# Performance work log

Hardware: AMD Instinct MI355X
Metric: run time of the kernel (lower is better)

Reference implementation:

```python
import jax, jax.numpy as jnp
import numpy as np

HEADS = 16

def _layernorm_LC(x, eps=1e-05):
    # Normalizes jointly over the last TWO dims (L, C), matching the custom LayerNorm.
    mean = jnp.mean(x, axis=(-2, -1), keepdims=True)
    var = jnp.mean((x - mean) ** 2, axis=(-2, -1), keepdims=True) + eps
    return (x - mean) / jnp.sqrt(var)  # affine is identity (ones/zeros)


def setup_inputs() -> dict:
    key = jax.random.key(0)
    ks = jax.random.split(key, 11)
    B, L, D = 2, 2048, 1024
    H = 4 * D
    s = 0.02
    return {
        'x': jax.random.normal(ks[0], (B, L, D), jnp.float32),
        'wq': jax.random.normal(ks[1], (D, D), jnp.float32) * s,
        'bq': jax.random.normal(ks[2], (D,), jnp.float32) * s,
        'wk': jax.random.normal(ks[3], (D, D), jnp.float32) * s,
        'bk': jax.random.normal(ks[4], (D,), jnp.float32) * s,
        'wv': jax.random.normal(ks[5], (D, D), jnp.float32) * s,
        'bv': jax.random.normal(ks[6], (D,), jnp.float32) * s,
        'w1': jax.random.normal(ks[7], (D, H), jnp.float32) * s,
        'b1': jax.random.normal(ks[8], (H,), jnp.float32) * s,
        'w2': jax.random.normal(ks[9], (H, D), jnp.float32) * s,
        'b2': jax.random.normal(ks[10], (D,), jnp.float32) * s,
    }


def reference(x, wq, bq, wk, bk, wv, bv, w1, b1, w2, b2):
    B, L, D = x.shape
    dh = D // HEADS
    # QKV projections
    q = (x @ wq + bq).reshape(B, L, HEADS, dh)
    k = (x @ wk + bk).reshape(B, L, HEADS, dh)
    v = (x @ wv + bv).reshape(B, L, HEADS, dh)
    # batched multi-head attention (equivalent to the per-head Python loop)
    scale = 1.0 / jnp.sqrt(jnp.float32(dh))
    scores = jnp.einsum('blhd,bmhd->bhlm', q, k) * scale
    attn = jax.nn.softmax(scores, axis=-1)
    out = jnp.einsum('bhlm,bmhd->blhd', attn, v).reshape(B, L, D)
    # residual + (L,C) layernorm
    h = _layernorm_LC(x + out)
    # feedforward (dropout is identity in eval)
    ff = jax.nn.relu(h @ w1 + b1) @ w2 + b2
    return _layernorm_LC(h + ff)
```

## Files before the change

### kernel.cpp

```cpp
#include <hip/hip_runtime.h>
#include <hip/hip_bf16.h>

typedef __hip_bfloat16 bf16;
typedef __attribute__((ext_vector_type(8))) short short8;
typedef __attribute__((ext_vector_type(4))) short short4v;
typedef __attribute__((ext_vector_type(4))) float f32x4;

#define CB 2
#define CL 2048
#define CD 1024
#define CH 4096
#define NHEADS 16
#define DH 64

__device__ __forceinline__ short f2bs(float f) {
    __hip_bfloat16 h = __float2bfloat16(f);
    return *reinterpret_cast<short*>(&h);
}
__device__ __forceinline__ float bs2f(short s) {
    __hip_bfloat16 h = *reinterpret_cast<__hip_bfloat16*>(&s);
    return __bfloat162float(h);
}

__device__ __forceinline__ void async_copy16(const short* g, short* l) {
    __builtin_amdgcn_global_load_lds((const __attribute__((address_space(1))) unsigned int*)g,
                                     (__attribute__((address_space(3))) unsigned int*)l,
                                     16, 0, 0);
}

__global__ void pack_bias_kernel(const float* __restrict__ bq, const float* __restrict__ bk,
                                 const float* __restrict__ bv, float* __restrict__ o,
                                 float* __restrict__ stats) {
    int i = blockIdx.x * 256 + threadIdx.x;
    if (i < 16) stats[i] = 0.0f;
    if (i < 3072) o[i] = i < 1024 ? bq[i] : (i < 2048 ? bk[i - 1024] : bv[i - 2048]);
}

__global__ void cvt_x_kernel(const float* __restrict__ x, short* __restrict__ o) {
    const int i = (blockIdx.x * 256 + threadIdx.x) * 4;
    const float4 v = *(const float4*)&x[i];
    short4v s; s[0] = f2bs(v.x); s[1] = f2bs(v.y); s[2] = f2bs(v.z); s[3] = f2bs(v.w);
    *(short4v*)&o[i] = s;
}

__global__ void transpose_cvt(const float* __restrict__ in, short* __restrict__ out,
                              int K, int N, int row_off) {
    __shared__ float T[32][33];
    const int tx = threadIdx.x & 31, ty = threadIdx.x >> 5;
    const int k0 = blockIdx.y * 32, n0 = blockIdx.x * 32;
    #pragma unroll
    for (int i = 0; i < 4; ++i)
        T[ty + i * 8][tx] = in[(size_t)(k0 + ty + i * 8) * N + n0 + tx];
    __syncthreads();
    #pragma unroll
    for (int i = 0; i < 4; ++i)
        out[(size_t)(row_off + n0 + ty + i * 8) * K + k0 + tx] = f2bs(T[tx][ty + i * 8]);
}

__global__ void transpose_qkv(const float* __restrict__ wq, const float* __restrict__ wk,
                              const float* __restrict__ wv, short* __restrict__ out) {
    __shared__ float T[32][33];
    const int z = blockIdx.z;
    const float* in = z == 0 ? wq : (z == 1 ? wk : wv);
    const int row_off = z * 1024;
    const int tx = threadIdx.x & 31, ty = threadIdx.x >> 5;
    const int k0 = blockIdx.y * 32, n0 = blockIdx.x * 32;
    #pragma unroll
    for (int i = 0; i < 4; ++i)
        T[ty + i * 8][tx] = in[(size_t)(k0 + ty + i * 8) * CD + n0 + tx];
    __syncthreads();
    #pragma unroll
    for (int i = 0; i < 4; ++i)
        out[(size_t)(row_off + n0 + ty + i * 8) * CD + k0 + tx] = f2bs(T[tx][ty + i * 8]);
}

template <int BN, int BK, int RELU, int EPI>
__launch_bounds__(256)
__global__ void gemm_mfma(const short* __restrict__ A,
                          const short* __restrict__ Bt,
                          const float* __restrict__ bias,
                          short* __restrict__ C,
                          short* __restrict__ C2,
                          int M, int N, int K,
                          float* __restrict__ stats) {
    constexpr int NT = BN / 32;
    constexpr int KH = BK / 32;
    constexpr int ACH = 16 * BK;
    constexpr int BCH = BN * BK / 8;
    __shared__ short As[128 * BK];
    __shared__ short Bs[BN * BK];
    __shared__ float red[8];

    const int tid = threadIdx.x;
    const int wave = tid >> 6, lane = tid & 63, quad = lane >> 4, lm = lane & 15;
    const int wm = (wave & 1) * 64, wn = (wave >> 1) * (NT * 16);

    const int id = blockIdx.y * gridDim.x + blockIdx.x;
    const int xcd = id & 7, within = id >> 3;
    const int by = xcd * 4 + (within & 3);
    const int bx = within >> 2;
    const int row0 = by * 128, col0 = bx * BN;

    f32x4 acc[4][NT];
    #pragma unroll
    for (int i = 0; i < 4; ++i)
        #pragma unroll
        for (int j = 0; j < NT; ++j) { f32x4 z = {0.f, 0.f, 0.f, 0.f}; acc[i][j] = z; }

    for (int k0 = 0; k0 < K; k0 += BK) {
        #pragma unroll
        for (int t = 0; t < ACH / 256; ++t) {
            const int c = t * 256 + tid;
            const int slab = c >> 9, idx = c & 511;
            const int r = idx >> 2, seg = idx & 3;
            async_copy16(A + (size_t)(row0 + r) * K + k0 + slab * 32 + seg * 8, &As[c * 8]);
        }
        #pragma unroll
        for (int t = 0; t < BCH / 256; ++t) {
            const int c = t * 256 + tid;
            const int slab = c / (BN * 4), idx = c % (BN * 4);
            const int r = idx >> 2, seg = idx & 3;
            async_copy16(Bt + (size_t)(col0 + r) * K + k0 + slab * 32 + seg * 8, &Bs[c * 8]);
        }
        __syncthreads();

        #pragma unroll
        for (int kh = 0; kh < KH; ++kh) {
            short8 af[4], bfr[NT];
            #pragma unroll
            for (int mt = 0; mt < 4; ++mt)
                af[mt] = *(const short8*)&As[kh * 4096 + (wm + mt * 16 + lm) * 32 + quad * 8];
            #pragma unroll
            for (int nt = 0; nt < NT; ++nt)
                bfr[nt] = *(const short8*)&Bs[kh * (BN * 32) + (wn + nt * 16 + lm) * 32 + quad * 8];
            #pragma unroll
            for (int mt = 0; mt < 4; ++mt)
                #pragma unroll
                for (int nt = 0; nt < NT; ++nt)
                    acc[mt][nt] = __builtin_amdgcn_mfma_f32_16x16x32_bf16(af[mt], bfr[nt], acc[mt][nt], 0, 0, 0);
        }
        __syncthreads();
    }

    float s1 = 0.f, s2 = 0.f;
    #pragma unroll
    for (int mt = 0; mt < 4; ++mt) {
        #pragma unroll
        for (int nt = 0; nt < NT; ++nt) {
            const int col = col0 + wn + nt * 16 + lm;
            const float bv = bias[col];
            const int rowb = row0 + wm + mt * 16 + quad * 4;
            if (EPI == 1 && col >= 2048) {
                const int b = row0 >> 11;
                const int l0 = rowb & (CL - 1);
                short4v sv;
                #pragma unroll
                for (int r = 0; r < 4; ++r) sv[r] = f2bs(acc[mt][nt][r] + bv);
                *(short4v*)&C2[(size_t)b * CD * CL + (size_t)(col - 2048) * CL + l0] = sv;
            } else {
                #pragma unroll
                for (int r = 0; r < 4; ++r) {
                    float v = acc[mt][nt][r] + bv;
                    if (RELU) v = fmaxf(v, 0.f);
                    const int ld = (EPI == 1) ? 2048 : N;
                    const size_t idx = (size_t)(rowb + r) * ld + col;
                    if (EPI == 2) {
                        v += bs2f(C[idx]);
                        s1 += v; s2 += v * v;
                    }
                    C[idx] = f2bs(v);
                }
            }
        }
    }
    if (EPI == 2) {
        #pragma unroll
        for (int off = 1; off <= 32; off <<= 1) {
            s1 += __shfl_xor(s1, off, 64);
            s2 += __shfl_xor(s2, off, 64);
        }
        if (lane == 0) { red[wave] = s1; red[4 + wave] = s2; }
        __syncthreads();
        if (tid == 0) {
            const int batch = row0 >> 11;
            atomicAdd(&stats[batch * 2 + 0], red[0] + red[1] + red[2] + red[3]);
            atomicAdd(&stats[batch * 2 + 1], red[4] + red[5] + red[6] + red[7]);
        }
    }
}

__launch_bounds__(256)
__global__ void attn_mfma(const short* __restrict__ qk,
                          const short* __restrict__ vT,
                          const float* __restrict__ x,
                          short* __restrict__ sbuf,
                          float* __restrict__ stats) {
    __shared__ short Ks[2][64 * 64];
    __shared__ short Vs[2][64 * 64];
    __shared__ float red[8];

    const int tid = threadIdx.x;
    const int wave = tid >> 6, lane = tid & 63, quad = lane >> 4, lm = lane & 15;
    const int sx = lm & 7;

    const int id = blockIdx.z * (16 * 16) + blockIdx.y * 16 + blockIdx.x;
    const int xcd = id & 7, rest = id >> 3;
    const int qx = rest & 15, gq = rest >> 4;
    const int g = gq * 8 + xcd;
    const int h = g & 15, b = g >> 4;

    const int hoff = h * DH;
    const size_t rowb = (size_t)b * CL;
    const size_t vbase = (size_t)b * CD * CL + (size_t)hoff * CL;
    const int qbase0 = qx * 128 + wave * 32;

    short8 bq[2][2];
    #pragma unroll
    for (int qt = 0; qt < 2; ++qt)
        #pragma unroll
        for (int kf = 0; kf < 2; ++kf)
            bq[qt][kf] = *(const short8*)(qk + (rowb + qbase0 + qt * 16 + lm) * 2048 + hoff + kf * 32 + quad * 8);

    f32x4 oacc[2][4];
    #pragma unroll
    for (int qt = 0; qt < 2; ++qt)
        #pragma unroll
        for (int mt = 0; mt < 4; ++mt) { f32x4 z = {0.f, 0.f, 0.f, 0.f}; oacc[qt][mt] = z; }
    float lsum[2] = {0.f, 0.f};

    auto stage = [&](int buf, int kt) {
        #pragma unroll
        for (int t = 0; t < 2; ++t) {
            const int c = tid + t * 256;
            const int key = c >> 3, sp = c & 7;
            async_copy16(qk + (rowb + kt * 64 + key) * 2048 + 1024 + hoff + ((sp ^ (key & 7)) * 8),
                         &Ks[buf][c * 8]);
        }
        #pragma unroll
        for (int t = 0; t < 2; ++t) {
            const int c = tid + t * 256;
            const int row = c >> 3, sp = c & 7;
            async_copy16(vT + vbase + (size_t)row * CL + kt * 64 + ((sp ^ (row & 7)) * 8),
                         &Vs[buf][c * 8]);
        }
    };

    stage(0, 0);
    __syncthreads();
    int cur = 0;

    for (int kt = 0; kt < CL / 64; ++kt) {
        if (kt + 1 < CL / 64) stage(cur ^ 1, kt + 1);
        const short* K_ = &Ks[cur][0];
        const short* V_ = &Vs[cur][0];

        float st[2][4][4];
        #pragma unroll
        for (int ktile = 0; ktile < 4; ++ktile) {
            const int krow = ktile * 16 + lm;
            const int s0 = (quad ^ sx) << 3;
            const short8 a0 = *(const short8*)&K_[krow * 64 + s0];
            const short8 a1 = *(const short8*)&K_[krow * 64 + (s0 ^ 32)];
            f32x4 sv[2];
            __builtin_amdgcn_s_setprio(1);
            #pragma unroll
            for (int qt = 0; qt < 2; ++qt) {
                f32x4 s = {0.f, 0.f, 0.f, 0.f};
                s = __builtin_amdgcn_mfma_f32_16x16x32_bf16(a0, bq[qt][0], s, 0, 0, 0);
                s = __builtin_amdgcn_mfma_f32_16x16x32_bf16(a1, bq[qt][1], s, 0, 0, 0);
                sv[qt] = s;
            }
            __builtin_amdgcn_s_setprio(0);
            #pragma unroll
            for (int qt = 0; qt < 2; ++qt)
                #pragma unroll
                for (int r = 0; r < 4; ++r) {
                    const float p = __expf(sv[qt][r] * 0.125f);
                    lsum[qt] += p;
                    st[qt][ktile][r] = p;
                }
        }

        #pragma unroll
        for (int p = 0; p < 2; ++p) {
            short8 pf[2];
            #pragma unroll
            for (int qt = 0; qt < 2; ++qt)
                #pragma unroll
                for (int r = 0; r < 4; ++r) {
                    pf[qt][r]     = f2bs(st[qt][2 * p][r]);
                    pf[qt][4 + r] = f2bs(st[qt][2 * p + 1][r]);
                }
            #pragma unroll
            for (int mt = 0; mt < 4; ++mt) {
                const int vrow = mt * 16 + lm;
                const int sc = (p * 4 + (quad >> 1)) ^ sx;
                const int vb = vrow * 64 + (quad & 1) * 4;
                const short4v vlo = *(const short4v*)&V_[vb + sc * 8];
                const short4v vhi = *(const short4v*)&V_[vb + (sc ^ 2) * 8];
                short8 vf;
                vf[0] = vlo[0]; vf[1] = vlo[1]; vf[2] = vlo[2]; vf[3] = vlo[3];
                vf[4] = vhi[0]; vf[5] = vhi[1]; vf[6] = vhi[2]; vf[7] = vhi[3];
                __builtin_amdgcn_s_setprio(1);
                #pragma unroll
                for (int qt = 0; qt < 2; ++qt)
                    oacc[qt][mt] = __builtin_amdgcn_mfma_f32_16x16x32_bf16(vf, pf[qt], oacc[qt][mt], 0, 0, 0);
                __builtin_amdgcn_s_setprio(0);
            }
        }
        __syncthreads();
        cur ^= 1;
    }

    #pragma unroll
    for (int qt = 0; qt < 2; ++qt) {
        lsum[qt] += __shfl_xor(lsum[qt], 16, 64);
        lsum[qt] += __shfl_xor(lsum[qt], 32, 64);
    }

    float s1 = 0.f, s2 = 0.f;
    #pragma unroll
    for (int qt = 0; qt < 2; ++qt) {
        const float inv = 1.0f / lsum[qt];
        const size_t grow = rowb + qbase0 + qt * 16 + lm;
        #pragma unroll
        for (int mt = 0; mt < 4; ++mt) {
            const size_t base = grow * CD + hoff + mt * 16 + quad * 4;
            const float4 xv = *(const float4*)&x[base];
            const float xa[4] = {xv.x, xv.y, xv.z, xv.w};
            short4v sv;
            #pragma unroll
            for (int r = 0; r < 4; ++r) {
                const float s = xa[r] + oacc[qt][mt][r] * inv;
                s1 += s; s2 += s * s;
                sv[r] = f2bs(s);
            }
            *(short4v*)&sbuf[base] = sv;
        }
    }
    #pragma unroll
    for (int off = 1; off <= 32; off <<= 1) {
        s1 += __shfl_xor(s1, off, 64);
        s2 += __shfl_xor(s2, off, 64);
    }
    if (lane == 0) { red[wave] = s1; red[4 + wave] = s2; }
    __syncthreads();
    if (tid == 0) {
        atomicAdd(&stats[b * 2 + 0], red[0] + red[1] + red[2] + red[3]);
        atomicAdd(&stats[b * 2 + 1], red[4] + red[5] + red[6] + red[7]);
    }
}

template <typename TO>
__global__ void ln_apply(const short* __restrict__ s, const float* __restrict__ stats,
                         TO* __restrict__ out, int perBatch) {
    const int bId = blockIdx.y;
    const size_t base = (size_t)bId * perBatch;
    const float n = (float)perBatch;
    const float mean = stats[bId * 2 + 0] / n;
    const float var  = stats[bId * 2 + 1] / n - mean * mean + 1e-5f;
    const float inv  = rsqrtf(var);
    const int stride = gridDim.x * 256 * 8;
    for (int i = (blockIdx.x * 256 + threadIdx.x) * 8; i < perBatch; i += stride) {
        const short8 v8 = *(const short8*)&s[base + i];
        float o[8];
        #pragma unroll
        for (int j = 0; j < 8; ++j) o[j] = (bs2f(v8[j]) - mean) * inv;
        if (sizeof(TO) == 4) {
            float4 f0 = {o[0], o[1], o[2], o[3]}, f1 = {o[4], o[5], o[6], o[7]};
            *(float4*)&((float*)out)[base + i] = f0;
            *(float4*)&((float*)out)[base + i + 4] = f1;
        } else {
            short8 r;
            #pragma unroll
            for (int j = 0; j < 8; ++j) r[j] = f2bs(o[j]);
            *(short8*)&((short*)out)[base + i] = r;
        }
    }
}

extern "C" void kernel_launch(void* const* d_in, const int* in_sizes, int n_in,
                              void* d_out, int out_size, void* d_ws, size_t ws_size,
                              hipStream_t stream) {
    const float* x  = (const float*)d_in[0];
    const float* wq = (const float*)d_in[1];
    const float* bq = (const float*)d_in[2];
    const float* wk = (const float*)d_in[3];
    const float* bk = (const float*)d_in[4];
    const float* wv = (const float*)d_in[5];
    const float* bv = (const float*)d_in[6];
    const float* w1 = (const float*)d_in[7];
    const float* b1 = (const float*)d_in[8];
    const float* w2 = (const float*)d_in[9];
    const float* b2 = (const float*)d_in[10];

    const int BL = CB * CL;
    const int perBatch = CL * CD;

    char* ws = (char*)d_ws;
    const size_t MB = 1024 * 1024;
    short* Wqkvt = (short*)(ws);
    float* bqkv  = (float*)(ws + 6 * MB);
    short* w1t   = (short*)(ws);
    short* w2t   = (short*)(ws);
    short* xbf   = (short*)(ws + 8 * MB);
    short* qkb   = (short*)(ws + 16 * MB);
    short* vT    = (short*)(ws + 32 * MB);
    short* ff1   = (short*)(ws + 8 * MB);
    short* hbuf  = (short*)(ws + 40 * MB);
    float* stats = (float*)(ws + 48 * MB);

    dim3 blk(256);

    pack_bias_kernel<<<12, blk, 0, stream>>>(bq, bk, bv, bqkv, stats);
    cvt_x_kernel<<<BL * CD / 1024, blk, 0, stream>>>(x, xbf);
    transpose_qkv<<<dim3(32, 32, 3), blk, 0, stream>>>(wq, wk, wv, Wqkvt);

    gemm_mfma<128, 64, 0, 1><<<dim3(3072 / 128, BL / 128), blk, 0, stream>>>(
        xbf, Wqkvt, bqkv, qkb, vT, BL, 3072, CD, nullptr);

    attn_mfma<<<dim3(CL / 128, NHEADS, CB), blk, 0, stream>>>(qkb, vT, x, hbuf, stats);

    ln_apply<bf16><<<dim3(128, CB), blk, 0, stream>>>(hbuf, stats, (bf16*)hbuf, perBatch);

    transpose_cvt<<<dim3(128, 32), blk, 0, stream>>>(w1, w1t, CD, CH, 0);
    gemm_mfma<128, 64, 1, 0><<<dim3(CH / 128, BL / 128), blk, 0, stream>>>(
        hbuf, w1t, b1, ff1, nullptr, BL, CH, CD, nullptr);

    transpose_cvt<<<dim3(32, 128), blk, 0, stream>>>(w2, w2t, CH, CD, 0);
    gemm_mfma<64, 128, 0, 2><<<dim3(CD / 64, BL / 128), blk, 0, stream>>>(
        ff1, w2t, b2, hbuf, nullptr, BL, CD, CH, stats + 8);

    ln_apply<float><<<dim3(128, CB), blk, 0, stream>>>(hbuf, stats + 8, (float*)d_out, perBatch);
}
```

Baseline: 349.0 us.

## Use 8 waves per attention block and permute V transpose for single-vector loads

The attention kernel goes from 4 waves handling 32 query rows each to 8 waves handling 16 rows each, which halves per-wave registers and raises the number of waves available to hide latency. The staging loop shrinks to one copy per thread for K and V, and the reduction buffer grows to cover 8 waves. The QKV GEMM epilogue now writes the transposed V with a permuted sequence index, so the attention kernel can load each V fragment with one 16-byte LDS read instead of two 8-byte reads plus shuffles. In exchange, each K/V tile loaded into LDS is shared across more waves that each do less MFMA work, so there is more sync overhead per unit of compute.

Result: no change. 345.6 us (-1.0%).

```diff
diff --git a/kernel.cpp b/kernel.cpp
--- a/kernel.cpp
+++ b/kernel.cpp
@@ -153,10 +153,11 @@
             if (EPI == 1 && col >= 2048) {
                 const int b = row0 >> 11;
                 const int l0 = rowb & (CL - 1);
+                const int lp = (l0 & ~63) | (l0 & 32) | ((l0 & 12) << 1) | ((l0 & 16) >> 2);
                 short4v sv;
                 #pragma unroll
                 for (int r = 0; r < 4; ++r) sv[r] = f2bs(acc[mt][nt][r] + bv);
-                *(short4v*)&C2[(size_t)b * CD * CL + (size_t)(col - 2048) * CL + l0] = sv;
+                *(short4v*)&C2[(size_t)b * CD * CL + (size_t)(col - 2048) * CL + lp] = sv;
             } else {
                 #pragma unroll
                 for (int r = 0; r < 4; ++r) {
@@ -189,7 +190,7 @@
     }
 }
 
-__launch_bounds__(256)
+__launch_bounds__(512)
 __global__ void attn_mfma(const short* __restrict__ qk,
                           const short* __restrict__ vT,
                           const float* __restrict__ x,
@@ -197,7 +198,7 @@
                           float* __restrict__ stats) {
     __shared__ short Ks[2][64 * 64];
     __shared__ short Vs[2][64 * 64];
-    __shared__ float red[8];
+    __shared__ float red[16];
 
     const int tid = threadIdx.x;
     const int wave = tid >> 6, lane = tid & 63, quad = lane >> 4, lm = lane & 15;
@@ -212,36 +213,28 @@
     const int hoff = h * DH;
     const size_t rowb = (size_t)b * CL;
     const size_t vbase = (size_t)b * CD * CL + (size_t)hoff * CL;
-    const int qbase0 = qx * 128 + wave * 32;
-
-    short8 bq[2][2];
-    #pragma unroll
-    for (int qt = 0; qt < 2; ++qt)
-        #pragma unroll
-        for (int kf = 0; kf < 2; ++kf)
-            bq[qt][kf] = *(const short8*)(qk + (rowb + qbase0 + qt * 16 + lm) * 2048 + hoff + kf * 32 + quad * 8);
-
-    f32x4 oacc[2][4];
-    #pragma unroll
-    for (int qt = 0; qt < 2; ++qt)
-        #pragma unroll
-        for (int mt = 0; mt < 4; ++mt) { f32x4 z = {0.f, 0.f, 0.f, 0.f}; oacc[qt][mt] = z; }
-    float lsum[2] = {0.f, 0.f};
+    const int qbase0 = qx * 128 + wave * 16;
+
+    short8 bq[2];
+    #pragma unroll
+    for (int kf = 0; kf < 2; ++kf)
+        bq[kf] = *(const short8*)(qk + (rowb + qbase0 + lm) * 2048 + hoff + kf * 32 + quad * 8);
+
+    f32x4 oacc[4];
+    #pragma unroll
+    for (int mt = 0; mt < 4; ++mt) { f32x4 z = {0.f, 0.f, 0.f, 0.f}; oacc[mt] = z; }
+    float lsum = 0.f;
 
     auto stage = [&](int buf, int kt) {
-        #pragma unroll
-        for (int t = 0; t < 2; ++t) {
-            const int c = tid + t * 256;
-            const int key = c >> 3, sp = c & 7;
+        {
+            const int key = tid >> 3, sp = tid & 7;
             async_copy16(qk + (rowb + kt * 64 + key) * 2048 + 1024 + hoff + ((sp ^ (key & 7)) * 8),
-                         &Ks[buf][c * 8]);
-        }
-        #pragma unroll
-        for (int t = 0; t < 2; ++t) {
-            const int c = tid + t * 256;
-            const int row = c >> 3, sp = c & 7;
+                         &Ks[buf][tid * 8]);
+        }
+        {
+            const int row = tid >> 3, sp = tid & 7;
             async_copy16(vT + vbase + (size_t)row * CL + kt * 64 + ((sp ^ (row & 7)) * 8),
-                         &Vs[buf][c * 8]);
+                         &Vs[buf][tid * 8]);
         }
     };
 
@@ -254,57 +247,40 @@
         const short* K_ = &Ks[cur][0];
         const short* V_ = &Vs[cur][0];
 
-        float st[2][4][4];
+        float st[4][4];
         #pragma unroll
         for (int ktile = 0; ktile < 4; ++ktile) {
             const int krow = ktile * 16 + lm;
             const int s0 = (quad ^ sx) << 3;
             const short8 a0 = *(const short8*)&K_[krow * 64 + s0];
             const short8 a1 = *(const short8*)&K_[krow * 64 + (s0 ^ 32)];
-            f32x4 sv[2];
+            f32x4 s = {0.f, 0.f, 0.f, 0.f};
             __builtin_amdgcn_s_setprio(1);
-            #pragma unroll
-            for (int qt = 0; qt < 2; ++qt) {
-                f32x4 s = {0.f, 0.f, 0.f, 0.f};
-                s = __builtin_amdgcn_mfma_f32_16x16x32_bf16(a0, bq[qt][0], s, 0, 0, 0);
-                s = __builtin_amdgcn_mfma_f32_16x16x32_bf16(a1, bq[qt][1], s, 0, 0, 0);
-                sv[qt] = s;
+            s = __builtin_amdgcn_mfma_f32_16x16x32_bf16(a0, bq[0], s, 0, 0, 0);
+            s = __builtin_amdgcn_mfma_f32_16x16x32_bf16(a1, bq[1], s, 0, 0, 0);
+            __builtin_amdgcn_s_setprio(0);
+            #pragma unroll
+            for (int r = 0; r < 4; ++r) {
+                const float p = __expf(s[r] * 0.125f);
+                lsum += p;
+                st[ktile][r] = p;
             }
-            __builtin_amdgcn_s_setprio(0);
-            #pragma unroll
-            for (int qt = 0; qt < 2; ++qt)
-                #pragma unroll
-                for (int r = 0; r < 4; ++r) {
-                    const float p = __expf(sv[qt][r] * 0.125f);
-                    lsum[qt] += p;
-                    st[qt][ktile][r] = p;
-                }
         }
 
         #pragma unroll
         for (int p = 0; p < 2; ++p) {
-            short8 pf[2];
-            #pragma unroll
-            for (int qt = 0; qt < 2; ++qt)
-                #pragma unroll
-                for (int r = 0; r < 4; ++r) {
-                    pf[qt][r]     = f2bs(st[qt][2 * p][r]);
-                    pf[qt][4 + r] = f2bs(st[qt][2 * p + 1][r]);
-                }
+            short8 pf;
+            #pragma unroll
+            for (int r = 0; r < 4; ++r) {
+                pf[r]     = f2bs(st[2 * p][r]);
+                pf[4 + r] = f2bs(st[2 * p + 1][r]);
+            }
             #pragma unroll
             for (int mt = 0; mt < 4; ++mt) {
-                const int vrow = mt * 16 + lm;
-                const int sc = (p * 4 + (quad >> 1)) ^ sx;
-                const int vb = vrow * 64 + (quad & 1) * 4;
-                const short4v vlo = *(const short4v*)&V_[vb + sc * 8];
-                const short4v vhi = *(const short4v*)&V_[vb + (sc ^ 2) * 8];
-                short8 vf;
-                vf[0] = vlo[0]; vf[1] = vlo[1]; vf[2] = vlo[2]; vf[3] = vlo[3];
-                vf[4] = vhi[0]; vf[5] = vhi[1]; vf[6] = vhi[2]; vf[7] = vhi[3];
+                const int sc = (p * 4 + quad) ^ sx;
+                const short8 vf = *(const short8*)&V_[(mt * 16 + lm) * 64 + sc * 8];
                 __builtin_amdgcn_s_setprio(1);
-                #pragma unroll
-                for (int qt = 0; qt < 2; ++qt)
-                    oacc[qt][mt] = __builtin_amdgcn_mfma_f32_16x16x32_bf16(vf, pf[qt], oacc[qt][mt], 0, 0, 0);
+                oacc[mt] = __builtin_amdgcn_mfma_f32_16x16x32_bf16(vf, pf, oacc[mt], 0, 0, 0);
                 __builtin_amdgcn_s_setprio(0);
             }
         }
@@ -312,17 +288,13 @@
         cur ^= 1;
     }
 
-    #pragma unroll
-    for (int qt = 0; qt < 2; ++qt) {
-        lsum[qt] += __shfl_xor(lsum[qt], 16, 64);
-        lsum[qt] += __shfl_xor(lsum[qt], 32, 64);
-    }
+    lsum += __shfl_xor(lsum, 16, 64);
+    lsum += __shfl_xor(lsum, 32, 64);
 
     float s1 = 0.f, s2 = 0.f;
-    #pragma unroll
-    for (int qt = 0; qt < 2; ++qt) {
-        const float inv = 1.0f / lsum[qt];
-        const size_t grow = rowb + qbase0 + qt * 16 + lm;
+    {
+        const float inv = 1.0f / lsum;
+        const size_t grow = rowb + qbase0 + lm;
         #pragma unroll
         for (int mt = 0; mt < 4; ++mt) {
             const size_t base = grow * CD + hoff + mt * 16 + quad * 4;
@@ -331,7 +303,7 @@
             short4v sv;
             #pragma unroll
             for (int r = 0; r < 4; ++r) {
-                const float s = xa[r] + oacc[qt][mt][r] * inv;
+                const float s = xa[r] + oacc[mt][r] * inv;
                 s1 += s; s2 += s * s;
                 sv[r] = f2bs(s);
             }
@@ -343,11 +315,14 @@
         s1 += __shfl_xor(s1, off, 64);
         s2 += __shfl_xor(s2, off, 64);
     }
-    if (lane == 0) { red[wave] = s1; red[4 + wave] = s2; }
+    if (lane == 0) { red[wave] = s1; red[8 + wave] = s2; }
     __syncthreads();
     if (tid == 0) {
-        atomicAdd(&stats[b * 2 + 0], red[0] + red[1] + red[2] + red[3]);
-        atomicAdd(&stats[b * 2 + 1], red[4] + red[5] + red[6] + red[7]);
+        float t1 = 0.f, t2 = 0.f;
+        #pragma unroll
+        for (int w = 0; w < 8; ++w) { t1 += red[w]; t2 += red[8 + w]; }
+        atomicAdd(&stats[b * 2 + 0], t1);
+        atomicAdd(&stats[b * 2 + 1], t2);
     }
 }
 
@@ -419,7 +394,7 @@
     gemm_mfma<128, 64, 0, 1><<<dim3(3072 / 128, BL / 128), blk, 0, stream>>>(
         xbf, Wqkvt, bqkv, qkb, vT, BL, 3072, CD, nullptr);
 
-    attn_mfma<<<dim3(CL / 128, NHEADS, CB), blk, 0, stream>>>(qkb, vT, x, hbuf, stats);
+    attn_mfma<<<dim3(CL / 128, NHEADS, CB), dim3(512), 0, stream>>>(qkb, vT, x, hbuf, stats);
 
     ln_apply<bf16><<<dim3(128, CB), blk, 0, stream>>>(hbuf, stats, (bf16*)hbuf, perBatch);
 
```
